# Performance work log

Hardware: AMD Instinct MI355X
Metric: run time of the kernel (lower is better)

The kernel has to match this reference:

```python
import jax, jax.numpy as jnp
import numpy as np

WS = 8        # window_size
HEAD_DIM = 32
KEYS = ["ln1_g", "ln1_b", "qkv_w", "qkv_b", "rpb", "proj_w", "proj_b",
        "ln2_g", "ln2_b", "w1", "b1", "w2", "b2"]


def _rel_bias(rpb, ws):
    # rpb: [h, 2ws-1, 2ws-1] -> bias [h, P, P] via relative coordinates
    coords = np.stack(np.meshgrid(np.arange(ws), np.arange(ws), indexing='ij'), -1).reshape(-1, 2)
    rel = coords[:, None, :] - coords[None, :, :] + ws - 1  # [P,P,2]
    return rpb[:, rel[..., 0], rel[..., 1]]


def _sw_mask(nh, nw, p, shift):
    # boolean mask [nW, P, P]; True = masked (cross-segment after cyclic shift)
    m = np.zeros((nh, nw, p, p, p, p), dtype=bool)
    s = p - shift
    m[-1, :, :s, :, s:, :] = True
    m[-1, :, s:, :, :s, :] = True
    m[:, -1, :, :s, :, s:] = True
    m[:, -1, :, s:, :, :s] = True
    return jnp.asarray(m.reshape(nh * nw, p * p, p * p))


def _ln(x, g, b):
    mu = x.mean(-1, keepdims=True)
    var = ((x - mu) ** 2).mean(-1, keepdims=True)
    return (x - mu) / jnp.sqrt(var + 1e-5) * g + b


def _wmsa(x, qkv_w, qkv_b, rpb, proj_w, proj_b, shifted):
    B, H, W, C = x.shape
    ws, hd = WS, HEAD_DIM
    h = C // hd
    shift = ws // 2
    if shifted:
        x = jnp.roll(x, (-shift, -shift), axis=(1, 2))
    nh, nw = H // ws, W // ws
    # window partition: [B, nW, P, C]
    xw = x.reshape(B, nh, ws, nw, ws, C).transpose(0, 1, 3, 2, 4, 5).reshape(B, nh * nw, ws * ws, C)
    qkv = xw @ qkv_w + qkv_b                               # [B,nW,P,3C]
    qkv = qkv.reshape(B, nh * nw, ws * ws, 3, h, hd)       # (3h,c) split -> first h heads = q
    q, k, v = qkv[..., 0, :, :], qkv[..., 1, :, :], qkv[..., 2, :, :]
    sim = jnp.einsum('bwphd,bwqhd->bhwpq', q, k) * (hd ** -0.5)
    sim = sim + _rel_bias(rpb, ws)[None, :, None]
    if shifted:
        mask = _sw_mask(nh, nw, ws, shift)                 # [nW,P,P]
        sim = jnp.where(mask[None, None], -jnp.inf, sim)
    probs = jax.nn.softmax(sim, axis=-1)
    out = jnp.einsum('bhwpq,bwqhd->bwphd', probs, v).reshape(B, nh * nw, ws * ws, C)
    out = out @ proj_w + proj_b
    out = out.reshape(B, nh, nw, ws, ws, C).transpose(0, 1, 3, 2, 4, 5).reshape(B, H, W, C)
    if shifted:
        out = jnp.roll(out, (shift, shift), axis=(1, 2))
    return out


def _block(x, p, shifted):
    x = x + _wmsa(_ln(x, p['ln1_g'], p['ln1_b']), p['qkv_w'], p['qkv_b'], p['rpb'],
                  p['proj_w'], p['proj_b'], shifted)
    y = _ln(x, p['ln2_g'], p['ln2_b'])
    y = jax.nn.gelu(y @ p['w1'] + p['b1'], approximate=False) @ p['w2'] + p['b2']
    return x + y


def setup_inputs() -> dict:
    B, C, H, W = 2, 192, 256, 256
    h = C // HEAD_DIM
    key = jax.random.key(0)
    ks = jax.random.split(key, 11)
    n = lambda k, shape: jax.random.normal(k, shape, jnp.float32) * 0.02
    inp = {"x": jax.random.normal(ks[0], (B, C, H, W), jnp.float32)}
    for i, pre in enumerate(("b1_", "b2_")):
        o = 1 + i * 5
        inp[pre + "ln1_g"] = jnp.ones((C,), jnp.float32)
        inp[pre + "ln1_b"] = jnp.zeros((C,), jnp.float32)
        inp[pre + "qkv_w"] = n(ks[o], (C, 3 * C))
        inp[pre + "qkv_b"] = jnp.zeros((3 * C,), jnp.float32)
        inp[pre + "rpb"] = n(ks[o + 1], (h, 2 * WS - 1, 2 * WS - 1))
        inp[pre + "proj_w"] = n(ks[o + 2], (C, C))
        inp[pre + "proj_b"] = jnp.zeros((C,), jnp.float32)
        inp[pre + "ln2_g"] = jnp.ones((C,), jnp.float32)
        inp[pre + "ln2_b"] = jnp.zeros((C,), jnp.float32)
        inp[pre + "w1"] = n(ks[o + 3], (C, 4 * C))
        inp[pre + "b1"] = jnp.zeros((4 * C,), jnp.float32)
        inp[pre + "w2"] = n(ks[o + 4], (4 * C, C))
        inp[pre + "b2"] = jnp.zeros((C,), jnp.float32)
    return inp


def reference(x, b1_ln1_g, b1_ln1_b, b1_qkv_w, b1_qkv_b, b1_rpb, b1_proj_w, b1_proj_b,
              b1_ln2_g, b1_ln2_b, b1_w1, b1_b1, b1_w2, b1_b2,
              b2_ln1_g, b2_ln1_b, b2_qkv_w, b2_qkv_b, b2_rpb, b2_proj_w, b2_proj_b,
              b2_ln2_g, b2_ln2_b, b2_w1, b2_b1, b2_w2, b2_b2):
    p1 = dict(zip(KEYS, (b1_ln1_g, b1_ln1_b, b1_qkv_w, b1_qkv_b, b1_rpb, b1_proj_w, b1_proj_b,
                         b1_ln2_g, b1_ln2_b, b1_w1, b1_b1, b1_w2, b1_b2)))
    p2 = dict(zip(KEYS, (b2_ln1_g, b2_ln1_b, b2_qkv_w, b2_qkv_b, b2_rpb, b2_proj_w, b2_proj_b,
                         b2_ln2_g, b2_ln2_b, b2_w1, b2_b1, b2_w2, b2_b2)))
    t = jnp.transpose(x, (0, 2, 3, 1))   # b c h w -> b h w c
    t = _block(t, p1, shifted=False)     # W block
    t = _block(t, p2, shifted=True)      # SW block
    return jnp.transpose(t, (0, 3, 1, 2))  # b h w c -> b c h w
```

## Files before the change

kernel.cpp:

```cpp
#include <hip/hip_runtime.h>
#include <math.h>

typedef unsigned short u16;
typedef u16 u16x8 __attribute__((ext_vector_type(8)));
typedef __bf16 bf16x8 __attribute__((ext_vector_type(8)));
typedef float f32x4 __attribute__((ext_vector_type(4)));

__device__ __forceinline__ u16 f2bf(float f) {
    union { float f; unsigned u; } v; v.f = f;
    unsigned r = v.u + 0x7fffu + ((v.u >> 16) & 1u);
    return (u16)(r >> 16);
}

__device__ __forceinline__ void gload16(const void* g, void* l) {
    __builtin_amdgcn_global_load_lds((const __attribute__((address_space(1))) void*)g,
                                     (__attribute__((address_space(3))) void*)l,
                                     16, 0, 0);
}

__device__ __forceinline__ float redsum16(float s) {
    s += __shfl_xor(s, 1, 64);
    s += __shfl_xor(s, 2, 64);
    s += __shfl_xor(s, 4, 64);
    s += __shfl_xor(s, 8, 64);
    return s;
}

__global__ __launch_bounds__(256) void tl_k(const float* __restrict__ in,
                                            const float* __restrict__ g,
                                            const float* __restrict__ b,
                                            float* __restrict__ xbuf,
                                            u16* __restrict__ lnbuf) {
    __shared__ float T[192][33];
    __shared__ float MU[32], RS[32];
    const int t = threadIdx.x;
    const int bid = blockIdx.x;
    const int bb = bid >> 11;
    const int s0 = (bid & 2047) * 32;
    const float* src = in + (size_t)bb * 192 * 65536 + s0;
    const int sx = t & 31, cg = t >> 5;
#pragma unroll
    for (int i = 0; i < 24; i++) {
        int c = cg + i * 8;
        T[c][sx] = src[(size_t)c * 65536 + sx];
    }
    __syncthreads();
    {
        const int tok = t >> 3, sub = t & 7;
        float s = 0.f;
#pragma unroll
        for (int i = 0; i < 24; i++) s += T[sub + i * 8][tok];
        s += __shfl_xor(s, 1, 64); s += __shfl_xor(s, 2, 64); s += __shfl_xor(s, 4, 64);
        float mu = s * (1.f / 192.f);
        float q = 0.f;
#pragma unroll
        for (int i = 0; i < 24; i++) { float d = T[sub + i * 8][tok] - mu; q += d * d; }
        q += __shfl_xor(q, 1, 64); q += __shfl_xor(q, 2, 64); q += __shfl_xor(q, 4, 64);
        if (sub == 0) { MU[tok] = mu; RS[tok] = rsqrtf(q * (1.f / 192.f) + 1e-5f); }
    }
    __syncthreads();
    const size_t tokG0 = (size_t)bb * 65536 + s0;
#pragma unroll
    for (int i = 0; i < 3; i++) {
        int chunk = i * 256 + t;
        int tk = chunk / 24;
        int c0 = (chunk - tk * 24) * 8;
        float mu = MU[tk], rs = RS[tk];
        f32x4 g0 = *(const f32x4*)&g[c0], g1 = *(const f32x4*)&g[c0 + 4];
        f32x4 b0 = *(const f32x4*)&b[c0], b1 = *(const f32x4*)&b[c0 + 4];
        u16x8 ov;
#pragma unroll
        for (int e = 0; e < 4; e++) ov[e] = f2bf((T[c0 + e][tk] - mu) * rs * g0[e] + b0[e]);
#pragma unroll
        for (int e = 0; e < 4; e++) ov[e + 4] = f2bf((T[c0 + 4 + e][tk] - mu) * rs * g1[e] + b1[e]);
        *(u16x8*)&lnbuf[(tokG0 + tk) * 192 + c0] = ov;
    }
#pragma unroll
    for (int i = 0; i < 6; i++) {
        int chunk = i * 256 + t;
        int tk = chunk / 48;
        int c0 = (chunk - tk * 48) * 4;
        f32x4 v;
#pragma unroll
        for (int e = 0; e < 4; e++) v[e] = T[c0 + e][tk];
        *(f32x4*)&xbuf[(tokG0 + tk) * 192 + c0] = v;
    }
}

__global__ __launch_bounds__(256) void transpose_out(const float* __restrict__ in,
                                                     float* __restrict__ out) {
    __shared__ float t[32][33];
    const int b = blockIdx.z;
    const int c0 = blockIdx.y * 32;
    const int s0 = blockIdx.x * 32;
    const int tx = threadIdx.x, ty = threadIdx.y;
    const float* src = in + (size_t)b * 65536 * 192;
    float* dst = out + (size_t)b * 192 * 65536;
#pragma unroll
    for (int k = 0; k < 4; k++)
        t[ty + k * 8][tx] = src[(size_t)(s0 + ty + k * 8) * 192 + c0 + tx];
    __syncthreads();
#pragma unroll
    for (int k = 0; k < 4; k++)
        dst[(size_t)(c0 + ty + k * 8) * 65536 + s0 + tx] = t[tx][ty + k * 8];
}

__global__ __launch_bounds__(256) void wtrans(const float* __restrict__ w,
                                              u16* __restrict__ wt, int K, int N) {
    int idx = blockIdx.x * 256 + threadIdx.x;
    if (idx >= K * N) return;
    int n = idx / K, k = idx % K;
    wt[idx] = f2bf(w[(size_t)k * N + n]);
}

template <int ACT>
__global__ __launch_bounds__(256, 4) void gemm_small(const u16* __restrict__ A,
                                                     const u16* __restrict__ Wt,
                                                     const float* __restrict__ bias,
                                                     u16* __restrict__ outb,
                                                     int N, int Nb) {
    __shared__ __align__(16) u16 Bs[64 * 192];
    const int t = threadIdx.x, l = t & 63, w = t >> 6;
    const int nwg = gridDim.x, q8 = nwg >> 3;
    const int wg = (blockIdx.x & 7) * q8 + (blockIdx.x >> 3);
    const int bn = wg % Nb, bm = wg / Nb;
    const size_t m0 = (size_t)bm * 128;
    const int n0 = bn * 64;
    const int lc = l & 15, lg = l >> 4;

#pragma unroll
    for (int r = 0; r < 6; r++) {
        int f = r * 2048 + t * 8;
        int row = f / 192;
        int c = ((f - row * 192) >> 3) ^ (row & 7);
        gload16(Wt + (size_t)(n0 + row) * 192 + c * 8, &Bs[f]);
    }
    const u16* ga = A + (m0 + w * 32 + lc) * 192 + lg * 8;
    bf16x8 af[6][2];
#pragma unroll
    for (int ks = 0; ks < 6; ks++)
#pragma unroll
        for (int tm = 0; tm < 2; tm++)
            af[ks][tm] = *(const bf16x8*)(ga + tm * 3072 + ks * 32);

    f32x4 acc[2][4] = {};
    __syncthreads();
#pragma unroll
    for (int ks = 0; ks < 6; ks++) {
        bf16x8 bfr[4];
#pragma unroll
        for (int tn = 0; tn < 4; tn++) {
            int row = tn * 16 + lc;
            int p = (ks * 4 + lg) ^ (row & 7);
            bfr[tn] = *(const bf16x8*)&Bs[row * 192 + p * 8];
        }
#pragma unroll
        for (int tm = 0; tm < 2; tm++)
#pragma unroll
            for (int tn = 0; tn < 4; tn++)
                acc[tm][tn] = __builtin_amdgcn_mfma_f32_16x16x32_bf16(af[ks][tm], bfr[tn],
                                                                     acc[tm][tn], 0, 0, 0);
    }
    float bv[4];
#pragma unroll
    for (int tn = 0; tn < 4; tn++) bv[tn] = bias[n0 + tn * 16 + lc];
    __syncthreads();
    u16* Ct = Bs;
#pragma unroll
    for (int tm = 0; tm < 2; tm++)
#pragma unroll
        for (int tn = 0; tn < 4; tn++)
#pragma unroll
            for (int r = 0; r < 4; r++) {
                int row = w * 32 + tm * 16 + (lg << 2) + r;
                float v = acc[tm][tn][r] + bv[tn];
                Ct[row * 72 + tn * 16 + lc] = f2bf(v);
            }
    __syncthreads();
#pragma unroll
    for (int i = 0; i < 4; i++) {
        int row = i * 32 + (t >> 3), seg = t & 7;
        *(u16x8*)&outb[(m0 + row) * (size_t)N + n0 + seg * 8] =
            *(const u16x8*)&Ct[row * 72 + seg * 8];
    }
}

template <int DO_LN>
__global__ __launch_bounds__(512, 4) void proj_mlp(const u16* __restrict__ A,
                                                   const u16* __restrict__ PWt,
                                                   const float* __restrict__ pbias,
                                                   const float* __restrict__ g2,
                                                   const float* __restrict__ bl2,
                                                   const u16* __restrict__ W1t,
                                                   const float* __restrict__ b1,
                                                   const u16* __restrict__ W2t,
                                                   const float* __restrict__ b2,
                                                   float* __restrict__ res,
                                                   const float* __restrict__ gn,
                                                   const float* __restrict__ bn,
                                                   u16* __restrict__ lnout) {
    __shared__ __align__(16) u16 SMEM[40960];
    u16* Bs   = SMEM;
    u16* ln2t = SMEM;
    u16* W1s  = SMEM + 24576;
    u16* W2s  = SMEM + 30720;
    u16* Is   = SMEM + 36864;
    const int t = threadIdx.x, l = t & 63, w = t >> 6;
    const int nwg = gridDim.x, q8 = nwg >> 3;
    const int wg = (blockIdx.x & 7) * q8 + (blockIdx.x >> 3);
    const size_t m0 = (size_t)wg * 128;
    const int lc = l & 15, lg = l >> 4;

    f32x4 acc2[12] = {};

#pragma unroll
    for (int r = 0; r < 9; r++) {
        int f = r * 4096 + t * 8;
        int row = f / 192;
        int c = ((f - row * 192) >> 3) ^ (row & 7);
        gload16(PWt + (size_t)row * 192 + c * 8, &Bs[f]);
    }
    {
        const u16* ga = A + (m0 + w * 16 + lc) * 192 + lg * 8;
        bf16x8 af[6];
#pragma unroll
        for (int ks = 0; ks < 6; ks++) af[ks] = *(const bf16x8*)(ga + ks * 32);

        __syncthreads();
#pragma unroll
        for (int ks = 0; ks < 6; ks++) {
#pragma unroll
            for (int grp = 0; grp < 3; grp++) {
                bf16x8 bfr[4];
#pragma unroll
                for (int tn = 0; tn < 4; tn++) {
                    int row = (grp * 4 + tn) * 16 + lc;
                    int p = (ks * 4 + lg) ^ (row & 7);
                    bfr[tn] = *(const bf16x8*)&Bs[row * 192 + p * 8];
                }
#pragma unroll
                for (int tn = 0; tn < 4; tn++)
                    acc2[grp * 4 + tn] = __builtin_amdgcn_mfma_f32_16x16x32_bf16(af[ks], bfr[tn],
                                                                                 acc2[grp * 4 + tn], 0, 0, 0);
            }
        }
        __syncthreads();

        float pbv[12], gv[12], bb[12];
#pragma unroll
        for (int tn = 0; tn < 12; tn++) {
            pbv[tn] = pbias[tn * 16 + lc];
            gv[tn] = g2[tn * 16 + lc];
            bb[tn] = bl2[tn * 16 + lc];
        }
#pragma unroll
        for (int r = 0; r < 4; r++) {
            int row = w * 16 + (lg << 2) + r;
            size_t base = (m0 + row) * 192;
            float v[12], s = 0.f;
#pragma unroll
            for (int tn = 0; tn < 12; tn++) {
                v[tn] = acc2[tn][r] + pbv[tn] + res[base + tn * 16 + lc];
                s += v[tn];
            }
            s = redsum16(s);
            float mu = s * (1.f / 192.f);
            float q = 0.f;
#pragma unroll
            for (int tn = 0; tn < 12; tn++) { float d = v[tn] - mu; q += d * d; }
            q = redsum16(q);
            float rstd = rsqrtf(q * (1.f / 192.f) + 1e-5f);
#pragma unroll
            for (int tn = 0; tn < 12; tn++) {
                acc2[tn][r] = v[tn];
                int col = tn * 16 + lc;
                float lnv = (v[tn] - mu) * rstd * gv[tn] + bb[tn];
                ln2t[row * 192 + (((col >> 3) ^ (row & 7)) << 3) + (col & 7)] = f2bf(lnv);
            }
        }
    }

#define STW1(c)                                                               \
    do {                                                                      \
        int f = t * 8;                                                        \
        int row = f / 192;                                                    \
        int cw = ((f - row * 192) >> 3) ^ (row & 7);                          \
        gload16(W1t + ((size_t)(c) * 32 + row) * 192 + cw * 8, &W1s[f]);      \
        if (t < 256) {                                                        \
            int f2 = (512 + t) * 8;                                           \
            int row2 = f2 / 192;                                              \
            int cw2 = ((f2 - row2 * 192) >> 3) ^ (row2 & 7);                  \
            gload16(W1t + ((size_t)(c) * 32 + row2) * 192 + cw2 * 8,          \
                    &W1s[f2]);                                                \
        }                                                                     \
    } while (0)
#define STW2(c)                                                               \
    do {                                                                      \
        int f = t * 8;                                                        \
        int row = f >> 5;                                                     \
        int cw = ((f >> 3) & 3) ^ ((row >> 1) & 3);                           \
        gload16(W2t + (size_t)row * 768 + (c) * 32 + cw * 8, &W2s[f]);        \
        if (t < 256) {                                                        \
            int f2 = (512 + t) * 8;                                           \
            int row2 = f2 >> 5;                                               \
            int cw2 = ((f2 >> 3) & 3) ^ ((row2 >> 1) & 3);                    \
            gload16(W2t + (size_t)row2 * 768 + (c) * 32 + cw2 * 8,            \
                    &W2s[f2]);                                                \
        }                                                                     \
    } while (0)

    STW1(0);
    STW2(0);
    __syncthreads();

    bf16x8 af[6];
    {
        int row = w * 16 + lc;
#pragma unroll
        for (int ks = 0; ks < 6; ks++) {
            int p = (ks * 4 + lg) ^ (row & 7);
            af[ks] = *(const bf16x8*)&ln2t[row * 192 + p * 8];
        }
    }
#pragma unroll 1
    for (int c = 0; c < 24; c++) {
        f32x4 a1[2] = {};
#pragma unroll
        for (int ks = 0; ks < 6; ks++) {
            bf16x8 bfr[2];
#pragma unroll
            for (int tn = 0; tn < 2; tn++) {
                int row = tn * 16 + lc;
                int p = (ks * 4 + lg) ^ (row & 7);
                bfr[tn] = *(const bf16x8*)&W1s[row * 192 + p * 8];
            }
#pragma unroll
            for (int tn = 0; tn < 2; tn++)
                a1[tn] = __builtin_amdgcn_mfma_f32_16x16x32_bf16(af[ks], bfr[tn],
                                                                 a1[tn], 0, 0, 0);
        }
        float b1v[2];
#pragma unroll
        for (int tn = 0; tn < 2; tn++) b1v[tn] = b1[c * 32 + tn * 16 + lc];
#pragma unroll
        for (int tn = 0; tn < 2; tn++)
#pragma unroll
            for (int r = 0; r < 4; r++) {
                int row = w * 16 + (lg << 2) + r;
                int col = tn * 16 + lc;
                float x = a1[tn][r] + b1v[tn];
                float u = x * x;
                float y = x * fmaf(-0.07136031f, u, -1.5957691f);
                float v = x * __builtin_amdgcn_rcpf(1.0f + __expf(y));
                int cw = (col >> 3) ^ ((row >> 1) & 3);
                Is[row * 32 + cw * 8 + (col & 7)] = f2bf(v);
            }
        __syncthreads();
        if (c < 23) STW1(c + 1);
        bf16x8 a2;
        {
            int row = w * 16 + lc;
            int ch = lg ^ ((row >> 1) & 3);
            a2 = *(const bf16x8*)&Is[row * 32 + ch * 8];
        }
#pragma unroll
        for (int grp = 0; grp < 2; grp++) {
            bf16x8 b2f[6];
#pragma unroll
            for (int tn = 0; tn < 6; tn++) {
                int row = (grp * 6 + tn) * 16 + lc;
                int ch = lg ^ ((row >> 1) & 3);
                b2f[tn] = *(const bf16x8*)&W2s[row * 32 + ch * 8];
            }
#pragma unroll
            for (int tn = 0; tn < 6; tn++)
                acc2[grp * 6 + tn] = __builtin_amdgcn_mfma_f32_16x16x32_bf16(a2, b2f[tn],
                                                                            acc2[grp * 6 + tn], 0, 0, 0);
        }
        __syncthreads();
        if (c < 23) STW2(c + 1);
    }
#undef STW1
#undef STW2
    float bv2[12];
#pragma unroll
    for (int tn = 0; tn < 12; tn++) bv2[tn] = b2[tn * 16 + lc];
    float gv2[12], bb2[12];
    if (DO_LN) {
#pragma unroll
        for (int tn = 0; tn < 12; tn++) { gv2[tn] = gn[tn * 16 + lc]; bb2[tn] = bn[tn * 16 + lc]; }
    }
#pragma unroll
    for (int r = 0; r < 4; r++) {
        int row = w * 16 + (lg << 2) + r;
        size_t base = (m0 + row) * 192;
        float v[12], s = 0.f;
#pragma unroll
        for (int tn = 0; tn < 12; tn++) {
            v[tn] = acc2[tn][r] + bv2[tn];
            s += v[tn];
        }
#pragma unroll
        for (int tn = 0; tn < 12; tn++) res[base + tn * 16 + lc] = v[tn];
        if (DO_LN) {
            s = redsum16(s);
            float mu = s * (1.f / 192.f);
            float q = 0.f;
#pragma unroll
            for (int tn = 0; tn < 12; tn++) { float d = v[tn] - mu; q += d * d; }
            q = redsum16(q);
            float rstd = rsqrtf(q * (1.f / 192.f) + 1e-5f);
#pragma unroll
            for (int tn = 0; tn < 12; tn++)
                lnout[base + tn * 16 + lc] = f2bf((v[tn] - mu) * rstd * gv2[tn] + bb2[tn]);
        }
    }
}

__global__ __launch_bounds__(64) void attn_k(const u16* __restrict__ qkv,
                                             const float* __restrict__ rpb,
                                             u16* __restrict__ aout, int shifted) {
    __shared__ __align__(16) u16 Vt[32][72];
    __shared__ __align__(16) u16 Ps[64][72];
    const int l = threadIdx.x;
    const int head = blockIdx.x;
    const int wy = blockIdx.y;
    const int b = wy >> 10, widx = wy & 1023;
    const int wh = widx >> 5, ww = widx & 31;
    const int soff = shifted ? 4 : 0;
    const int lc = l & 15;
    const int lg = l >> 4;

    {
        int i1 = l >> 3, j1 = l & 7;
        int hh = (wh * 8 + i1 + soff) & 255;
        int wc = (ww * 8 + j1 + soff) & 255;
        const u16* base = qkv + (((size_t)b * 256 + hh) * 256 + wc) * 576 + head * 32 + 384;
#pragma unroll
        for (int s = 0; s < 4; s++) {
            u16x8 v = *(const u16x8*)(base + s * 8);
#pragma unroll
            for (int e = 0; e < 8; e++) Vt[s * 8 + e][l] = v[e];
        }
    }

    bf16x8 qa[4], kb[4];
#pragma unroll
    for (int tm = 0; tm < 4; tm++) {
        int p = tm * 16 + lc;
        int pi = p >> 3, pj = p & 7;
        int hh = (wh * 8 + pi + soff) & 255;
        int wc = (ww * 8 + pj + soff) & 255;
        const u16* tp = qkv + (((size_t)b * 256 + hh) * 256 + wc) * 576 + head * 32;
        qa[tm] = *(const bf16x8*)(tp + lg * 8);
        kb[tm] = *(const bf16x8*)(tp + 192 + lg * 8);
    }

    f32x4 acc[4][4] = {};
    __builtin_amdgcn_s_setprio(1);
#pragma unroll
    for (int tm = 0; tm < 4; tm++)
#pragma unroll
        for (int tn = 0; tn < 4; tn++)
            acc[tm][tn] = __builtin_amdgcn_mfma_f32_16x16x32_bf16(qa[tm], kb[tn], acc[tm][tn], 0, 0, 0);
    __builtin_amdgcn_s_setprio(0);

    const float scale = 0.17677669529663687f;
    const float* rp = rpb + head * 225;
#pragma unroll
    for (int tm = 0; tm < 4; tm++) {
#pragma unroll
        for (int r = 0; r < 4; r++) {
            int p = tm * 16 + (lg << 2) + r;
            int pi = p >> 3, pj = p & 7;
            float sv[4];
#pragma unroll
            for (int tn = 0; tn < 4; tn++) {
                int qq = tn * 16 + lc;
                int qi = qq >> 3, qj = qq & 7;
                float xv = acc[tm][tn][r] * scale + rp[(pi - qi + 7) * 15 + (pj - qj + 7)];
                if (shifted) {
                    bool msk = (wh == 31 && ((pi < 4) != (qi < 4))) ||
                               (ww == 31 && ((pj < 4) != (qj < 4)));
                    if (msk) xv = -1e30f;
                }
                sv[tn] = xv;
            }
            float mx = fmaxf(fmaxf(sv[0], sv[1]), fmaxf(sv[2], sv[3]));
#pragma unroll
            for (int m = 1; m < 16; m <<= 1) mx = fmaxf(mx, __shfl_xor(mx, m, 64));
            float sum = 0.f;
#pragma unroll
            for (int tn = 0; tn < 4; tn++) { sv[tn] = __expf(sv[tn] - mx); sum += sv[tn]; }
#pragma unroll
            for (int m = 1; m < 16; m <<= 1) sum += __shfl_xor(sum, m, 64);
            float inv = 1.0f / sum;
#pragma unroll
            for (int tn = 0; tn < 4; tn++) Ps[p][tn * 16 + lc] = f2bf(sv[tn] * inv);
        }
    }
    __syncthreads();

    f32x4 o[4][2] = {};
    {
        bf16x8 pa[4], vb[2];
#pragma unroll
        for (int kk = 0; kk < 2; kk++) {
#pragma unroll
            for (int tm = 0; tm < 4; tm++) pa[tm] = *(const bf16x8*)&Ps[tm * 16 + lc][kk * 32 + lg * 8];
#pragma unroll
            for (int tn = 0; tn < 2; tn++) vb[tn] = *(const bf16x8*)&Vt[tn * 16 + lc][kk * 32 + lg * 8];
            __builtin_amdgcn_s_setprio(1);
#pragma unroll
            for (int tm = 0; tm < 4; tm++)
#pragma unroll
                for (int tn = 0; tn < 2; tn++)
                    o[tm][tn] = __builtin_amdgcn_mfma_f32_16x16x32_bf16(pa[tm], vb[tn], o[tm][tn], 0, 0, 0);
            __builtin_amdgcn_s_setprio(0);
        }
    }
#pragma unroll
    for (int tm = 0; tm < 4; tm++)
#pragma unroll
        for (int r = 0; r < 4; r++) {
            int p = tm * 16 + (lg << 2) + r;
            int pi = p >> 3, pj = p & 7;
            int h2 = (wh * 8 + pi + soff) & 255;
            int w2 = (ww * 8 + pj + soff) & 255;
            size_t t2 = ((size_t)b * 256 + h2) * 256 + w2;
#pragma unroll
            for (int tn = 0; tn < 2; tn++)
                aout[t2 * 192 + head * 32 + tn * 16 + lc] = f2bf(o[tm][tn][r]);
        }
}

extern "C" void kernel_launch(void* const* d_in, const int* in_sizes, int n_in,
                              void* d_out, int out_size, void* d_ws, size_t ws_size,
                              hipStream_t stream) {
    (void)in_sizes; (void)n_in; (void)out_size; (void)ws_size;
    const float* x_in = (const float*)d_in[0];

    char* ws = (char*)d_ws;
    float* xbuf = (float*)ws;
    u16* lnbuf = (u16*)(ws + 100663296);
    u16* big   = (u16*)(ws + 150994944);
    u16* wts   = (u16*)(ws + 352321536);

    u16* qkvt[2]; u16* projt[2]; u16* w1t[2]; u16* w2t[2];
    for (int bi = 0; bi < 2; bi++) {
        size_t base = (size_t)bi * 442368;
        qkvt[bi]  = wts + base;
        projt[bi] = wts + base + 110592;
        w1t[bi]   = wts + base + 147456;
        w2t[bi]   = wts + base + 294912;
    }

    for (int bi = 0; bi < 2; bi++) {
        const int base = 1 + bi * 13;
        wtrans<<<dim3((110592 + 255) / 256), 256, 0, stream>>>((const float*)d_in[base + 2],  qkvt[bi],  192, 576);
        wtrans<<<dim3((36864  + 255) / 256), 256, 0, stream>>>((const float*)d_in[base + 5],  projt[bi], 192, 192);
        wtrans<<<dim3((147456 + 255) / 256), 256, 0, stream>>>((const float*)d_in[base + 9],  w1t[bi],   192, 768);
        wtrans<<<dim3((147456 + 255) / 256), 256, 0, stream>>>((const float*)d_in[base + 11], w2t[bi],   768, 192);
    }

    tl_k<<<4096, 256, 0, stream>>>(x_in, (const float*)d_in[1], (const float*)d_in[2], xbuf, lnbuf);

    for (int bi = 0; bi < 2; bi++) {
        const int base = 1 + bi * 13;
        const float* qkv_b  = (const float*)d_in[base + 3];
        const float* rpb    = (const float*)d_in[base + 4];
        const float* proj_b = (const float*)d_in[base + 6];
        const float* ln2_g  = (const float*)d_in[base + 7];
        const float* ln2_b  = (const float*)d_in[base + 8];
        const float* b1     = (const float*)d_in[base + 10];
        const float* b2     = (const float*)d_in[base + 12];

        gemm_small<0><<<9216, 256, 0, stream>>>(lnbuf, qkvt[bi], qkv_b, big, 576, 9);
        attn_k<<<dim3(6, 2048), 64, 0, stream>>>(big, rpb, lnbuf, bi);
        if (bi == 0) {
            proj_mlp<1><<<1024, 512, 0, stream>>>(lnbuf, projt[bi], proj_b, ln2_g, ln2_b,
                                                  w1t[bi], b1, w2t[bi], b2, xbuf,
                                                  (const float*)d_in[14], (const float*)d_in[15], lnbuf);
        } else {
            proj_mlp<0><<<1024, 512, 0, stream>>>(lnbuf, projt[bi], proj_b, ln2_g, ln2_b,
                                                  w1t[bi], b1, w2t[bi], b2, xbuf,
                                                  nullptr, nullptr, nullptr);
        }
    }

    transpose_out<<<dim3(2048, 6, 2), dim3(32, 8), 0, stream>>>(xbuf, (float*)d_out);
}
```

Measured before the change: 724.1 us.

## Fuse QKV projection GEMM into per-window attention kernel

Replaces the separate QKV GEMM and attention kernels with one kernel per window that loads the 64 shifted-window tokens into LDS and computes Q, K, V per head with MFMA. It then runs attention in place and writes the output to a new buffer. This drops the round trip of the large 576-wide QKV intermediate through global memory and one launch. In exchange, QKV weights are read directly from global memory by every block with no LDS staging. Heads are processed serially, with several barriers per head.

```diff
diff --git a/kernel.cpp b/kernel.cpp
--- a/kernel.cpp
+++ b/kernel.cpp
@@ -113,75 +113,146 @@
     wt[idx] = f2bf(w[(size_t)k * N + n]);
 }
 
-template <int ACT>
-__global__ __launch_bounds__(256, 4) void gemm_small(const u16* __restrict__ A,
-                                                     const u16* __restrict__ Wt,
-                                                     const float* __restrict__ bias,
-                                                     u16* __restrict__ outb,
-                                                     int N, int Nb) {
-    __shared__ __align__(16) u16 Bs[64 * 192];
+__global__ __launch_bounds__(256) void qkv_attn(const u16* __restrict__ lnb,
+                                                const u16* __restrict__ Wt,
+                                                const float* __restrict__ qb,
+                                                const float* __restrict__ rpb,
+                                                u16* __restrict__ aout, int shifted) {
+    __shared__ __align__(16) u16 SMEM[12288];
+    u16* As = SMEM;
+    u16* Qs = SMEM;
+    u16* Ks = SMEM + 2560;
+    u16* Vt = SMEM + 5120;
+    u16* Ps = SMEM + 7424;
     const int t = threadIdx.x, l = t & 63, w = t >> 6;
-    const int nwg = gridDim.x, q8 = nwg >> 3;
-    const int wg = (blockIdx.x & 7) * q8 + (blockIdx.x >> 3);
-    const int bn = wg % Nb, bm = wg / Nb;
-    const size_t m0 = (size_t)bm * 128;
-    const int n0 = bn * 64;
+    const int wy = blockIdx.x;
+    const int b = wy >> 10, widx = wy & 1023;
+    const int wh = widx >> 5, ww = widx & 31;
+    const int soff = shifted ? 4 : 0;
     const int lc = l & 15, lg = l >> 4;
 
 #pragma unroll
-    for (int r = 0; r < 6; r++) {
-        int f = r * 2048 + t * 8;
-        int row = f / 192;
-        int c = ((f - row * 192) >> 3) ^ (row & 7);
-        gload16(Wt + (size_t)(n0 + row) * 192 + c * 8, &Bs[f]);
-    }
-    const u16* ga = A + (m0 + w * 32 + lc) * 192 + lg * 8;
-    bf16x8 af[6][2];
-#pragma unroll
-    for (int ks = 0; ks < 6; ks++)
-#pragma unroll
-        for (int tm = 0; tm < 2; tm++)
-            af[ks][tm] = *(const bf16x8*)(ga + tm * 3072 + ks * 32);
-
-    f32x4 acc[2][4] = {};
+    for (int i = 0; i < 6; i++) {
+        int cid = i * 256 + t;
+        int row = cid / 24, cc = cid - row * 24;
+        int hh = (wh * 8 + (row >> 3) + soff) & 255;
+        int wc = (ww * 8 + (row & 7) + soff) & 255;
+        size_t tok = ((size_t)b * 256 + hh) * 256 + wc;
+        gload16(lnb + tok * 192 + (size_t)(cc ^ (row & 7)) * 8, &As[cid * 8]);
+    }
     __syncthreads();
-#pragma unroll
-    for (int ks = 0; ks < 6; ks++) {
-        bf16x8 bfr[4];
-#pragma unroll
-        for (int tn = 0; tn < 4; tn++) {
-            int row = tn * 16 + lc;
+    bf16x8 af[6];
+    {
+        int row = w * 16 + lc;
+#pragma unroll
+        for (int ks = 0; ks < 6; ks++) {
             int p = (ks * 4 + lg) ^ (row & 7);
-            bfr[tn] = *(const bf16x8*)&Bs[row * 192 + p * 8];
-        }
-#pragma unroll
-        for (int tm = 0; tm < 2; tm++)
+            af[ks] = *(const bf16x8*)&As[row * 192 + p * 8];
+        }
+    }
+    __syncthreads();
+
+    const float scale = 0.17677669529663687f;
+    const int prow = w * 16 + (lg << 2);
+#pragma unroll 1
+    for (int head = 0; head < 6; head++) {
+        f32x4 acc[6] = {};
+#pragma unroll
+        for (int ks = 0; ks < 6; ks++) {
+            bf16x8 bfr[6];
+#pragma unroll
+            for (int j = 0; j < 6; j++) {
+                int nrow = (j >> 1) * 192 + head * 32 + (j & 1) * 16 + lc;
+                bfr[j] = *(const bf16x8*)&Wt[(size_t)nrow * 192 + ks * 32 + lg * 8];
+            }
+#pragma unroll
+            for (int j = 0; j < 6; j++)
+                acc[j] = __builtin_amdgcn_mfma_f32_16x16x32_bf16(af[ks], bfr[j], acc[j], 0, 0, 0);
+        }
+        float bv[6];
+#pragma unroll
+        for (int j = 0; j < 6; j++)
+            bv[j] = qb[(j >> 1) * 192 + head * 32 + (j & 1) * 16 + lc];
+#pragma unroll
+        for (int j = 0; j < 6; j++)
+#pragma unroll
+            for (int r = 0; r < 4; r++) {
+                int row = prow + r;
+                int col = (j & 1) * 16 + lc;
+                u16 v = f2bf(acc[j][r] + bv[j]);
+                if (j < 2) Qs[row * 40 + col] = v;
+                else if (j < 4) Ks[row * 40 + col] = v;
+                else Vt[col * 72 + row] = v;
+            }
+        __syncthreads();
+
+        f32x4 sacc[4] = {};
+        {
+            bf16x8 qa = *(const bf16x8*)&Qs[(w * 16 + lc) * 40 + lg * 8];
+            bf16x8 kb[4];
 #pragma unroll
             for (int tn = 0; tn < 4; tn++)
-                acc[tm][tn] = __builtin_amdgcn_mfma_f32_16x16x32_bf16(af[ks][tm], bfr[tn],
-                                                                     acc[tm][tn], 0, 0, 0);
-    }
-    float bv[4];
-#pragma unroll
-    for (int tn = 0; tn < 4; tn++) bv[tn] = bias[n0 + tn * 16 + lc];
-    __syncthreads();
-    u16* Ct = Bs;
-#pragma unroll
-    for (int tm = 0; tm < 2; tm++)
-#pragma unroll
-        for (int tn = 0; tn < 4; tn++)
-#pragma unroll
-            for (int r = 0; r < 4; r++) {
-                int row = w * 32 + tm * 16 + (lg << 2) + r;
-                float v = acc[tm][tn][r] + bv[tn];
-                Ct[row * 72 + tn * 16 + lc] = f2bf(v);
-            }
-    __syncthreads();
-#pragma unroll
-    for (int i = 0; i < 4; i++) {
-        int row = i * 32 + (t >> 3), seg = t & 7;
-        *(u16x8*)&outb[(m0 + row) * (size_t)N + n0 + seg * 8] =
-            *(const u16x8*)&Ct[row * 72 + seg * 8];
+                kb[tn] = *(const bf16x8*)&Ks[(tn * 16 + lc) * 40 + lg * 8];
+#pragma unroll
+            for (int tn = 0; tn < 4; tn++)
+                sacc[tn] = __builtin_amdgcn_mfma_f32_16x16x32_bf16(qa, kb[tn], sacc[tn], 0, 0, 0);
+        }
+        const float* rp = rpb + head * 225;
+#pragma unroll
+        for (int r = 0; r < 4; r++) {
+            int p = prow + r;
+            int pi = p >> 3, pj = p & 7;
+            float sv[4];
+#pragma unroll
+            for (int tn = 0; tn < 4; tn++) {
+                int qq = tn * 16 + lc;
+                int qi = qq >> 3, qj = qq & 7;
+                float xv = sacc[tn][r] * scale + rp[(pi - qi + 7) * 15 + (pj - qj + 7)];
+                if (shifted) {
+                    bool msk = (wh == 31 && ((pi < 4) != (qi < 4))) ||
+                               (ww == 31 && ((pj < 4) != (qj < 4)));
+                    if (msk) xv = -1e30f;
+                }
+                sv[tn] = xv;
+            }
+            float mx = fmaxf(fmaxf(sv[0], sv[1]), fmaxf(sv[2], sv[3]));
+#pragma unroll
+            for (int m = 1; m < 16; m <<= 1) mx = fmaxf(mx, __shfl_xor(mx, m, 64));
+            float sum = 0.f;
+#pragma unroll
+            for (int tn = 0; tn < 4; tn++) { sv[tn] = __expf(sv[tn] - mx); sum += sv[tn]; }
+#pragma unroll
+            for (int m = 1; m < 16; m <<= 1) sum += __shfl_xor(sum, m, 64);
+            float inv = 1.0f / sum;
+#pragma unroll
+            for (int tn = 0; tn < 4; tn++) Ps[p * 72 + tn * 16 + lc] = f2bf(sv[tn] * inv);
+        }
+        __syncthreads();
+
+        f32x4 o[2] = {};
+#pragma unroll
+        for (int kk = 0; kk < 2; kk++) {
+            bf16x8 pa = *(const bf16x8*)&Ps[(w * 16 + lc) * 72 + kk * 32 + lg * 8];
+            bf16x8 vb[2];
+#pragma unroll
+            for (int tn = 0; tn < 2; tn++)
+                vb[tn] = *(const bf16x8*)&Vt[(tn * 16 + lc) * 72 + kk * 32 + lg * 8];
+#pragma unroll
+            for (int tn = 0; tn < 2; tn++)
+                o[tn] = __builtin_amdgcn_mfma_f32_16x16x32_bf16(pa, vb[tn], o[tn], 0, 0, 0);
+        }
+#pragma unroll
+        for (int r = 0; r < 4; r++) {
+            int p = prow + r;
+            int pi = p >> 3, pj = p & 7;
+            int h2 = (wh * 8 + pi + soff) & 255;
+            int w2 = (ww * 8 + pj + soff) & 255;
+            size_t t2 = ((size_t)b * 256 + h2) * 256 + w2;
+#pragma unroll
+            for (int tn = 0; tn < 2; tn++)
+                aout[t2 * 192 + head * 32 + tn * 16 + lc] = f2bf(o[tn][r]);
+        }
+        __syncthreads();
     }
 }
 
@@ -417,123 +488,6 @@
     }
 }
 
-__global__ __launch_bounds__(64) void attn_k(const u16* __restrict__ qkv,
-                                             const float* __restrict__ rpb,
-                                             u16* __restrict__ aout, int shifted) {
-    __shared__ __align__(16) u16 Vt[32][72];
-    __shared__ __align__(16) u16 Ps[64][72];
-    const int l = threadIdx.x;
-    const int head = blockIdx.x;
-    const int wy = blockIdx.y;
-    const int b = wy >> 10, widx = wy & 1023;
-    const int wh = widx >> 5, ww = widx & 31;
-    const int soff = shifted ? 4 : 0;
-    const int lc = l & 15;
-    const int lg = l >> 4;
-
-    {
-        int i1 = l >> 3, j1 = l & 7;
-        int hh = (wh * 8 + i1 + soff) & 255;
-        int wc = (ww * 8 + j1 + soff) & 255;
-        const u16* base = qkv + (((size_t)b * 256 + hh) * 256 + wc) * 576 + head * 32 + 384;
-#pragma unroll
-        for (int s = 0; s < 4; s++) {
-            u16x8 v = *(const u16x8*)(base + s * 8);
-#pragma unroll
-            for (int e = 0; e < 8; e++) Vt[s * 8 + e][l] = v[e];
-        }
-    }
-
-    bf16x8 qa[4], kb[4];
-#pragma unroll
-    for (int tm = 0; tm < 4; tm++) {
-        int p = tm * 16 + lc;
-        int pi = p >> 3, pj = p & 7;
-        int hh = (wh * 8 + pi + soff) & 255;
-        int wc = (ww * 8 + pj + soff) & 255;
-        const u16* tp = qkv + (((size_t)b * 256 + hh) * 256 + wc) * 576 + head * 32;
-        qa[tm] = *(const bf16x8*)(tp + lg * 8);
-        kb[tm] = *(const bf16x8*)(tp + 192 + lg * 8);
-    }
-
-    f32x4 acc[4][4] = {};
-    __builtin_amdgcn_s_setprio(1);
-#pragma unroll
-    for (int tm = 0; tm < 4; tm++)
-#pragma unroll
-        for (int tn = 0; tn < 4; tn++)
-            acc[tm][tn] = __builtin_amdgcn_mfma_f32_16x16x32_bf16(qa[tm], kb[tn], acc[tm][tn], 0, 0, 0);
-    __builtin_amdgcn_s_setprio(0);
-
-    const float scale = 0.17677669529663687f;
-    const float* rp = rpb + head * 225;
-#pragma unroll
-    for (int tm = 0; tm < 4; tm++) {
-#pragma unroll
-        for (int r = 0; r < 4; r++) {
-            int p = tm * 16 + (lg << 2) + r;
-            int pi = p >> 3, pj = p & 7;
-            float sv[4];
-#pragma unroll
-            for (int tn = 0; tn < 4; tn++) {
-                int qq = tn * 16 + lc;
-                int qi = qq >> 3, qj = qq & 7;
-                float xv = acc[tm][tn][r] * scale + rp[(pi - qi + 7) * 15 + (pj - qj + 7)];
-                if (shifted) {
-                    bool msk = (wh == 31 && ((pi < 4) != (qi < 4))) ||
-                               (ww == 31 && ((pj < 4) != (qj < 4)));
-                    if (msk) xv = -1e30f;
-                }
-                sv[tn] = xv;
-            }
-            float mx = fmaxf(fmaxf(sv[0], sv[1]), fmaxf(sv[2], sv[3]));
-#pragma unroll
-            for (int m = 1; m < 16; m <<= 1) mx = fmaxf(mx, __shfl_xor(mx, m, 64));
-            float sum = 0.f;
-#pragma unroll
-            for (int tn = 0; tn < 4; tn++) { sv[tn] = __expf(sv[tn] - mx); sum += sv[tn]; }
-#pragma unroll
-            for (int m = 1; m < 16; m <<= 1) sum += __shfl_xor(sum, m, 64);
-            float inv = 1.0f / sum;
-#pragma unroll
-            for (int tn = 0; tn < 4; tn++) Ps[p][tn * 16 + lc] = f2bf(sv[tn] * inv);
-        }
-    }
-    __syncthreads();
-
-    f32x4 o[4][2] = {};
-    {
-        bf16x8 pa[4], vb[2];
-#pragma unroll
-        for (int kk = 0; kk < 2; kk++) {
-#pragma unroll
-            for (int tm = 0; tm < 4; tm++) pa[tm] = *(const bf16x8*)&Ps[tm * 16 + lc][kk * 32 + lg * 8];
-#pragma unroll
-            for (int tn = 0; tn < 2; tn++) vb[tn] = *(const bf16x8*)&Vt[tn * 16 + lc][kk * 32 + lg * 8];
-            __builtin_amdgcn_s_setprio(1);
-#pragma unroll
-            for (int tm = 0; tm < 4; tm++)
-#pragma unroll
-                for (int tn = 0; tn < 2; tn++)
-                    o[tm][tn] = __builtin_amdgcn_mfma_f32_16x16x32_bf16(pa[tm], vb[tn], o[tm][tn], 0, 0, 0);
-            __builtin_amdgcn_s_setprio(0);
-        }
-    }
-#pragma unroll
-    for (int tm = 0; tm < 4; tm++)
-#pragma unroll
-        for (int r = 0; r < 4; r++) {
-            int p = tm * 16 + (lg << 2) + r;
-            int pi = p >> 3, pj = p & 7;
-            int h2 = (wh * 8 + pi + soff) & 255;
-            int w2 = (ww * 8 + pj + soff) & 255;
-            size_t t2 = ((size_t)b * 256 + h2) * 256 + w2;
-#pragma unroll
-            for (int tn = 0; tn < 2; tn++)
-                aout[t2 * 192 + head * 32 + tn * 16 + lc] = f2bf(o[tm][tn][r]);
-        }
-}
-
 extern "C" void kernel_launch(void* const* d_in, const int* in_sizes, int n_in,
                               void* d_out, int out_size, void* d_ws, size_t ws_size,
                               hipStream_t stream) {
@@ -543,7 +497,7 @@
     char* ws = (char*)d_ws;
     float* xbuf = (float*)ws;
     u16* lnbuf = (u16*)(ws + 100663296);
-    u16* big   = (u16*)(ws + 150994944);
+    u16* abuf  = (u16*)(ws + 150994944);
     u16* wts   = (u16*)(ws + 352321536);
 
     u16* qkvt[2]; u16* projt[2]; u16* w1t[2]; u16* w2t[2];
@@ -575,14 +529,13 @@
         const float* b1     = (const float*)d_in[base + 10];
         const float* b2     = (const float*)d_in[base + 12];
 
-        gemm_small<0><<<9216, 256, 0, stream>>>(lnbuf, qkvt[bi], qkv_b, big, 576, 9);
-        attn_k<<<dim3(6, 2048), 64, 0, stream>>>(big, rpb, lnbuf, bi);
+        qkv_attn<<<2048, 256, 0, stream>>>(lnbuf, qkvt[bi], qkv_b, rpb, abuf, bi);
         if (bi == 0) {
-            proj_mlp<1><<<1024, 512, 0, stream>>>(lnbuf, projt[bi], proj_b, ln2_g, ln2_b,
+            proj_mlp<1><<<1024, 512, 0, stream>>>(abuf, projt[bi], proj_b, ln2_g, ln2_b,
                                                   w1t[bi], b1, w2t[bi], b2, xbuf,
                                                   (const float*)d_in[14], (const float*)d_in[15], lnbuf);
         } else {
-            proj_mlp<0><<<1024, 512, 0, stream>>>(lnbuf, projt[bi], proj_b, ln2_g, ln2_b,
+            proj_mlp<0><<<1024, 512, 0, stream>>>(abuf, projt[bi], proj_b, ln2_g, ln2_b,
                                                   w1t[bi], b1, w2t[bi], b2, xbuf,
                                                   nullptr, nullptr, nullptr);
         }
```

Result: slower. 894.4 us (+23.5%).
